# Kernel optimization log

Hardware: AMD Instinct MI355X
Metric: run time of the kernel (lower is better)

The kernel has to match this reference:

```python
import jax, jax.numpy as jnp
import numpy as np

EPS = 1e-8

def setup_inputs() -> dict:
    key = jax.random.key(0)
    k1, k2 = jax.random.split(key)
    B, N, D, K = 8, 8192, 768, 256
    x = jax.random.normal(k1, (B, N, D), dtype=jnp.float32)
    centers = jax.random.normal(k2, (B, K, D), dtype=jnp.float32)
    return {"x": x, "centers": centers}

def reference(x, centers):
    # tokens_norm / centers_norm as in the torch module (add-eps normalization)
    tn = x / (jnp.linalg.norm(x, axis=-1, keepdims=True) + EPS)
    cn = centers / (jnp.linalg.norm(centers, axis=-1, keepdims=True) + EPS)
    # F.cosine_similarity re-normalizes with clamp(norm, min=eps)
    tn2 = tn / jnp.maximum(jnp.linalg.norm(tn, axis=-1, keepdims=True), EPS)
    cn2 = cn / jnp.maximum(jnp.linalg.norm(cn, axis=-1, keepdims=True), EPS)
    # fused: cosine similarity via plain matmul instead of (B,N,K,D) broadcast
    cos_sim = jnp.einsum('bnd,bkd->bnk', tn2, cn2)  # (B,N,K)
    dist = 1.0 - cos_sim
    prob = jax.nn.softmax(-dist, axis=-1)  # softmax over K
    # weighted aggregation over N: (B,K,D)
    num = jnp.einsum('bnk,bnd->bkd', prob, x)
    den = jnp.sum(prob, axis=1)[..., None] + EPS  # (B,K,1)
    return num / den
```

## Files before the change

kernel.cpp:

```cpp
#include <hip/hip_runtime.h>
#include <hip/hip_bf16.h>

typedef __attribute__((ext_vector_type(8))) short bf16x8;
typedef __attribute__((ext_vector_type(4))) float f32x4;
typedef unsigned short u16;
typedef unsigned int u32;

__device__ __forceinline__ u16 f2bf(float f) {
    u32 u = __float_as_uint(f);
    u = (u + 0x7FFFu + ((u >> 16) & 1u)) >> 16;
    return (u16)u;
}
__device__ __forceinline__ u32 pk2(float a, float b) {
    return (u32)f2bf(a) | ((u32)f2bf(b) << 16);
}

#define GLDS16(g, l) __builtin_amdgcn_global_load_lds( \
    (const __attribute__((address_space(1))) u32*)(g), \
    (__attribute__((address_space(3))) u32*)(l), 16, 0, 0)

__global__ __launch_bounds__(256) void k_centers(const float* __restrict__ c, u16* __restrict__ cn,
                                                 float* __restrict__ den, float* __restrict__ out) {
    int bid = blockIdx.x;
    int w = threadIdx.x >> 6, lane = threadIdx.x & 63;
    int row = (bid << 2) + w;
    int b = row >> 8;
    if (bid < 8) den[(bid << 8) + threadIdx.x] = 0.f;
    {
        float4* o4 = reinterpret_cast<float4*>(out) + (size_t)bid * 768 + threadIdx.x;
        o4[0] = float4{0.f, 0.f, 0.f, 0.f};
        o4[256] = float4{0.f, 0.f, 0.f, 0.f};
        o4[512] = float4{0.f, 0.f, 0.f, 0.f};
    }
    __shared__ u16 rb[4][800];
    const float* src = c + (size_t)row * 768;
    float v[12]; float ss = 0.f;
#pragma unroll
    for (int j = 0; j < 12; ++j) { v[j] = src[lane + (j << 6)]; ss += v[j] * v[j]; }
#pragma unroll
    for (int m = 1; m < 64; m <<= 1) ss += __shfl_xor(ss, m, 64);
    float inv = 1.0f / sqrtf(ss);
#pragma unroll
    for (int j = 0; j < 12; ++j) rb[w][lane + (j << 6)] = f2bf(v[j] * inv);
    __syncthreads();
    int t = threadIdx.x;
    int k0 = (bid << 2) & 255;
#pragma unroll
    for (int p = 0; p < 2; ++p) {
        int idx = (p << 8) + t;
        if (idx < 384) {
            int g = idx >> 2, kr = idx & 3;
            uint4 val = *reinterpret_cast<const uint4*>(&rb[kr][g << 3]);
            int kb = g >> 2, dc = g & 3;
            size_t o = ((((size_t)(b * 24 + kb) << 2) + dc) << 8) + k0 + kr;
            *reinterpret_cast<uint4*>(cn + (o << 3)) = val;
        }
    }
}

__global__ __launch_bounds__(256, 2) void k_gemm1(const float* __restrict__ x, const u16* __restrict__ cn,
                                                  u16* __restrict__ probT, float* __restrict__ den) {
    const int b = blockIdx.y;
    const int n0 = blockIdx.x << 7;
    const int t = threadIdx.x;
    const int wave = t >> 6, lane = t & 63;
    const int lg = lane >> 4, lr = lane & 15;
    const int wm = wave >> 1, wk = wave & 1;
    const int tok0 = wm << 6;
    const int kb0 = wk << 7;

    __shared__ union {
        struct {
            u16 A[2][4][130][8];
            u16 B[2][4][256][8];
        } s;
        u16 T[256][136];
    } u;
    __shared__ float inv_s[128];
    __shared__ float ksum[2][128];
    __shared__ float denp[256];

    denp[t] = 0.f;

    f32x4 acc[8][4];
#pragma unroll
    for (int kf = 0; kf < 8; ++kf)
#pragma unroll
        for (int tf = 0; tf < 4; ++tf) acc[kf][tf] = (f32x4){0.f, 0.f, 0.f, 0.f};

    const char* cnb = (const char*)(cn + (size_t)b * 24 * 4 * 256 * 8);
    const int tokS = ((t >> 1) & 63) + ((t >> 7) << 6);
    const int dcS = t & 1;
    const float* ap = x + ((size_t)b * 8192 + n0 + tokS) * 768 + (dcS << 3);

    float sq = 0.f;
    float4 f0, f1, f2, f3;

    auto issueA = [&](int kb) {
        const float* p = ap + (kb << 5);
        f0 = *reinterpret_cast<const float4*>(p);
        f1 = *reinterpret_cast<const float4*>(p + 4);
        f2 = *reinterpret_cast<const float4*>(p + 16);
        f3 = *reinterpret_cast<const float4*>(p + 20);
    };
    auto writeA = [&](int buf) {
        sq += f0.x*f0.x + f0.y*f0.y + f0.z*f0.z + f0.w*f0.w
            + f1.x*f1.x + f1.y*f1.y + f1.z*f1.z + f1.w*f1.w
            + f2.x*f2.x + f2.y*f2.y + f2.z*f2.z + f2.w*f2.w
            + f3.x*f3.x + f3.y*f3.y + f3.z*f3.z + f3.w*f3.w;
        *reinterpret_cast<uint4*>(&u.s.A[buf][dcS][tokS][0]) =
            make_uint4(pk2(f0.x, f0.y), pk2(f0.z, f0.w), pk2(f1.x, f1.y), pk2(f1.z, f1.w));
        *reinterpret_cast<uint4*>(&u.s.A[buf][dcS + 2][tokS][0]) =
            make_uint4(pk2(f2.x, f2.y), pk2(f2.z, f2.w), pk2(f3.x, f3.y), pk2(f3.z, f3.w));
    };
    auto issueB = [&](int buf, int kb) {
        const char* src = cnb + (size_t)kb * 16384 + (wave << 12) + (lane << 4);
        char* dst = (char*)&u.s.B[buf][0][0][0] + (wave << 12);
        GLDS16(src, dst);
        GLDS16(src + 1024, dst + 1024);
        GLDS16(src + 2048, dst + 2048);
        GLDS16(src + 3072, dst + 3072);
    };

    issueA(0); issueB(0, 0);
    writeA(0);
    __syncthreads();

    for (int kb = 0; kb < 24; ++kb) {
        int cur = kb & 1, nxt = cur ^ 1;
        if (kb < 23) { issueA(kb + 1); issueB(nxt, kb + 1); }
        bf16x8 a[4];
#pragma unroll
        for (int tf = 0; tf < 4; ++tf)
            a[tf] = *reinterpret_cast<const bf16x8*>(&u.s.A[cur][lg][tok0 + (tf << 4) + lr][0]);
#pragma unroll
        for (int kf = 0; kf < 8; ++kf) {
            bf16x8 bb = *reinterpret_cast<const bf16x8*>(&u.s.B[cur][lg][kb0 + (kf << 4) + lr][0]);
#pragma unroll
            for (int tf = 0; tf < 4; ++tf)
                acc[kf][tf] = __builtin_amdgcn_mfma_f32_16x16x32_bf16(a[tf], bb, acc[kf][tf], 0, 0, 0);
        }
        if (kb < 23) writeA(nxt);
        __syncthreads();
    }

    sq += __shfl_xor(sq, 1, 64);
    if ((t & 1) == 0) inv_s[tokS] = 1.0f / sqrtf(sq);
    __syncthreads();

    float iv[4][4];
#pragma unroll
    for (int tf = 0; tf < 4; ++tf)
#pragma unroll
        for (int r = 0; r < 4; ++r)
            iv[tf][r] = inv_s[tok0 + (tf << 4) + (lg << 2) + r];

    float rowsum[4][4];
#pragma unroll
    for (int tf = 0; tf < 4; ++tf)
#pragma unroll
        for (int r = 0; r < 4; ++r) rowsum[tf][r] = 0.f;
#pragma unroll
    for (int kf = 0; kf < 8; ++kf)
#pragma unroll
        for (int tf = 0; tf < 4; ++tf)
#pragma unroll
            for (int r = 0; r < 4; ++r) {
                float e = __expf(acc[kf][tf][r] * iv[tf][r]);
                acc[kf][tf][r] = e; rowsum[tf][r] += e;
            }
#pragma unroll
    for (int tf = 0; tf < 4; ++tf)
#pragma unroll
        for (int r = 0; r < 4; ++r) {
#pragma unroll
            for (int m = 1; m < 16; m <<= 1) rowsum[tf][r] += __shfl_xor(rowsum[tf][r], m, 64);
        }
    if (lr == 0) {
#pragma unroll
        for (int tf = 0; tf < 4; ++tf)
#pragma unroll
            for (int r = 0; r < 4; ++r)
                ksum[wk][tok0 + (tf << 4) + (lg << 2) + r] = rowsum[tf][r];
    }
    __syncthreads();

    float rs[4][4];
#pragma unroll
    for (int tf = 0; tf < 4; ++tf)
#pragma unroll
        for (int r = 0; r < 4; ++r) {
            int idx = tok0 + (tf << 4) + (lg << 2) + r;
            rs[tf][r] = 1.0f / (ksum[0][idx] + ksum[1][idx]);
        }

    float dcol[8];
#pragma unroll
    for (int kf = 0; kf < 8; ++kf) dcol[kf] = 0.f;
#pragma unroll
    for (int kf = 0; kf < 8; ++kf)
#pragma unroll
        for (int tf = 0; tf < 4; ++tf)
#pragma unroll
            for (int r = 0; r < 4; ++r) {
                float p = acc[kf][tf][r] * rs[tf][r];
                acc[kf][tf][r] = p; dcol[kf] += p;
            }
#pragma unroll
    for (int kf = 0; kf < 8; ++kf) {
        dcol[kf] += __shfl_xor(dcol[kf], 16, 64);
        dcol[kf] += __shfl_xor(dcol[kf], 32, 64);
    }
    if (lg == 0) {
#pragma unroll
        for (int kf = 0; kf < 8; ++kf) atomicAdd(&denp[kb0 + (kf << 4) + lr], dcol[kf]);
    }
#pragma unroll
    for (int kf = 0; kf < 8; ++kf)
#pragma unroll
        for (int tf = 0; tf < 4; ++tf)
            *reinterpret_cast<ushort4*>(&u.T[kb0 + (kf << 4) + lr][tok0 + (tf << 4) + (lg << 2)]) =
                make_ushort4(f2bf(acc[kf][tf][0]), f2bf(acc[kf][tf][1]),
                             f2bf(acc[kf][tf][2]), f2bf(acc[kf][tf][3]));
    __syncthreads();

    u16* pTb = probT + (size_t)b * 256 * 8192 + n0;
#pragma unroll
    for (int i = 0; i < 16; ++i) {
        int idx = (i << 8) + t;
        int row = idx >> 4, ch = idx & 15;
        *reinterpret_cast<uint4*>(pTb + (size_t)row * 8192 + (ch << 3)) =
            *reinterpret_cast<const uint4*>(&u.T[row][ch << 3]);
    }
    atomicAdd(&den[(b << 8) + t], denp[t]);
}

__global__ __launch_bounds__(256) void k_gemm2(const float* __restrict__ x, const u16* __restrict__ probT,
                                               const float* __restrict__ den, float* __restrict__ out) {
    const int bid = blockIdx.x;
    const int xcd = bid & 7, slot = bid >> 3;
    const int orig = xcd * 96 + slot;
    const int dt = orig % 12, sb = orig / 12;
    const int s = sb >> 3, b = sb & 7;
    const int d0 = dt << 6;
    const int t = threadIdx.x;
    const int wave = t >> 6, lane = t & 63;
    const int lg = lane >> 4, lr = lane & 15;

    f32x4 acc[4][4];
#pragma unroll
    for (int m = 0; m < 4; ++m)
#pragma unroll
        for (int tt = 0; tt < 4; ++tt) acc[m][tt] = (f32x4){0.f, 0.f, 0.f, 0.f};

    const int n0 = s << 10;
    const u16* pA = probT + (size_t)b * 256 * 8192;
    const float* xB = x + (size_t)b * 8192 * 768;

    for (int kb = 0; kb < 32; ++kb) {
        int nbase = n0 + (kb << 5);
        bf16x8 a[4];
#pragma unroll
        for (int m = 0; m < 4; ++m) {
            int k = (wave << 6) + (m << 4) + lr;
            a[m] = *reinterpret_cast<const bf16x8*>(pA + (size_t)k * 8192 + nbase + (lg << 3));
        }
        const float* xr = xB + (size_t)(nbase + (lg << 3)) * 768 + d0 + lr;
        bf16x8 bb[4];
#pragma unroll
        for (int tt = 0; tt < 4; ++tt)
#pragma unroll
            for (int j = 0; j < 8; ++j) {
                float f = xr[(size_t)j * 768 + (tt << 4)];
                bb[tt][j] = (short)f2bf(f);
            }
#pragma unroll
        for (int m = 0; m < 4; ++m)
#pragma unroll
            for (int tt = 0; tt < 4; ++tt)
                acc[m][tt] = __builtin_amdgcn_mfma_f32_16x16x32_bf16(a[m], bb[tt], acc[m][tt], 0, 0, 0);
    }

    float* ob = out + (size_t)(b << 8) * 768;
#pragma unroll
    for (int m = 0; m < 4; ++m) {
        int kb_ = (wave << 6) + (m << 4) + (lg << 2);
#pragma unroll
        for (int reg = 0; reg < 4; ++reg) {
            float dv = 1.0f / (den[(b << 8) + kb_ + reg] + 1e-8f);
#pragma unroll
            for (int tt = 0; tt < 4; ++tt)
                unsafeAtomicAdd(&ob[(size_t)(kb_ + reg) * 768 + d0 + (tt << 4) + lr],
                                acc[m][tt][reg] * dv);
        }
    }
}

extern "C" void kernel_launch(void* const* d_in, const int* in_sizes, int n_in,
                              void* d_out, int out_size, void* d_ws, size_t ws_size,
                              hipStream_t stream) {
    const float* x = (const float*)d_in[0];
    const float* centers = (const float*)d_in[1];
    float* out = (float*)d_out;
    char* ws = (char*)d_ws;
    u16* cn       = (u16*)ws;
    u16* probT    = (u16*)(ws + 3145728);
    float* den    = (float*)(ws + 36700160);

    k_centers<<<512, 256, 0, stream>>>(centers, cn, den, out);
    k_gemm1<<<dim3(64, 8), 256, 0, stream>>>(x, cn, probT, den);
    k_gemm2<<<768, 256, 0, stream>>>(x, probT, den, out);
}
```

Before: 164.4 us.

## Replace double-buffered GEMM1 main loop with single-buffer 64-wide K steps

The 24-step double-buffered loop, which prefetched the next x tile and centers tile while computing the current one, is replaced by 12 single-buffered steps covering 64 elements of D each. Both LDS buffers now hold the two halves of one step. Each step loads 8 float4 per thread, stores them to LDS, synchronizes, then runs twice as many MFMAs per barrier. This halves the number of loop iterations and barriers and the x loads become wider and contiguous, but the overlap between global loads and MFMA work inside a block is lost. The kernel now relies on its two resident blocks per CU to hide load latency.

Measured after the change: 159.8 us (median of 2 runs). -2.8%, faster.

```diff
diff --git a/kernel.cpp b/kernel.cpp
--- a/kernel.cpp
+++ b/kernel.cpp
@@ -71,7 +71,7 @@
 
     __shared__ union {
         struct {
-            u16 A[2][4][130][8];
+            u16 A[8][130][8];
             u16 B[2][4][256][8];
         } s;
         u16 T[256][136];
@@ -91,56 +91,51 @@
     const char* cnb = (const char*)(cn + (size_t)b * 24 * 4 * 256 * 8);
     const int tokS = ((t >> 1) & 63) + ((t >> 7) << 6);
     const int dcS = t & 1;
-    const float* ap = x + ((size_t)b * 8192 + n0 + tokS) * 768 + (dcS << 3);
+    const float* ap = x + ((size_t)b * 8192 + n0 + tokS) * 768 + (dcS << 5);
 
     float sq = 0.f;
-    float4 f0, f1, f2, f3;
-
-    auto issueA = [&](int kb) {
-        const float* p = ap + (kb << 5);
-        f0 = *reinterpret_cast<const float4*>(p);
-        f1 = *reinterpret_cast<const float4*>(p + 4);
-        f2 = *reinterpret_cast<const float4*>(p + 16);
-        f3 = *reinterpret_cast<const float4*>(p + 20);
-    };
-    auto writeA = [&](int buf) {
-        sq += f0.x*f0.x + f0.y*f0.y + f0.z*f0.z + f0.w*f0.w
-            + f1.x*f1.x + f1.y*f1.y + f1.z*f1.z + f1.w*f1.w
-            + f2.x*f2.x + f2.y*f2.y + f2.z*f2.z + f2.w*f2.w
-            + f3.x*f3.x + f3.y*f3.y + f3.z*f3.z + f3.w*f3.w;
-        *reinterpret_cast<uint4*>(&u.s.A[buf][dcS][tokS][0]) =
-            make_uint4(pk2(f0.x, f0.y), pk2(f0.z, f0.w), pk2(f1.x, f1.y), pk2(f1.z, f1.w));
-        *reinterpret_cast<uint4*>(&u.s.A[buf][dcS + 2][tokS][0]) =
-            make_uint4(pk2(f2.x, f2.y), pk2(f2.z, f2.w), pk2(f3.x, f3.y), pk2(f3.z, f3.w));
-    };
-    auto issueB = [&](int buf, int kb) {
-        const char* src = cnb + (size_t)kb * 16384 + (wave << 12) + (lane << 4);
-        char* dst = (char*)&u.s.B[buf][0][0][0] + (wave << 12);
-        GLDS16(src, dst);
-        GLDS16(src + 1024, dst + 1024);
-        GLDS16(src + 2048, dst + 2048);
-        GLDS16(src + 3072, dst + 3072);
-    };
-
-    issueA(0); issueB(0, 0);
-    writeA(0);
-    __syncthreads();
-
-    for (int kb = 0; kb < 24; ++kb) {
-        int cur = kb & 1, nxt = cur ^ 1;
-        if (kb < 23) { issueA(kb + 1); issueB(nxt, kb + 1); }
-        bf16x8 a[4];
-#pragma unroll
-        for (int tf = 0; tf < 4; ++tf)
-            a[tf] = *reinterpret_cast<const bf16x8*>(&u.s.A[cur][lg][tok0 + (tf << 4) + lr][0]);
+
+    for (int it = 0; it < 12; ++it) {
+        const float* p = ap + (it << 6);
+        float4 f[8];
+#pragma unroll
+        for (int j = 0; j < 8; ++j) f[j] = *reinterpret_cast<const float4*>(p + (j << 2));
+#pragma unroll
+        for (int h = 0; h < 2; ++h) {
+            const char* src = cnb + (size_t)((it << 1) + h) * 16384 + (wave << 12) + (lane << 4);
+            char* dst = (char*)&u.s.B[h][0][0][0] + (wave << 12);
+            GLDS16(src, dst);
+            GLDS16(src + 1024, dst + 1024);
+            GLDS16(src + 2048, dst + 2048);
+            GLDS16(src + 3072, dst + 3072);
+        }
+#pragma unroll
+        for (int j = 0; j < 8; ++j)
+            sq += f[j].x * f[j].x + f[j].y * f[j].y + f[j].z * f[j].z + f[j].w * f[j].w;
+#pragma unroll
+        for (int j = 0; j < 4; ++j) {
+            *reinterpret_cast<uint4*>(&u.s.A[(dcS << 2) + j][tokS][0]) =
+                make_uint4(pk2(f[2 * j].x, f[2 * j].y), pk2(f[2 * j].z, f[2 * j].w),
+                           pk2(f[2 * j + 1].x, f[2 * j + 1].y), pk2(f[2 * j + 1].z, f[2 * j + 1].w));
+        }
+        __syncthreads();
+
+        bf16x8 a[4][2];
+#pragma unroll
+        for (int tf = 0; tf < 4; ++tf)
+#pragma unroll
+            for (int h = 0; h < 2; ++h)
+                a[tf][h] = *reinterpret_cast<const bf16x8*>(&u.s.A[(h << 2) + lg][tok0 + (tf << 4) + lr][0]);
 #pragma unroll
         for (int kf = 0; kf < 8; ++kf) {
-            bf16x8 bb = *reinterpret_cast<const bf16x8*>(&u.s.B[cur][lg][kb0 + (kf << 4) + lr][0]);
-#pragma unroll
-            for (int tf = 0; tf < 4; ++tf)
-                acc[kf][tf] = __builtin_amdgcn_mfma_f32_16x16x32_bf16(a[tf], bb, acc[kf][tf], 0, 0, 0);
-        }
-        if (kb < 23) writeA(nxt);
+#pragma unroll
+            for (int h = 0; h < 2; ++h) {
+                bf16x8 bb = *reinterpret_cast<const bf16x8*>(&u.s.B[h][lg][kb0 + (kf << 4) + lr][0]);
+#pragma unroll
+                for (int tf = 0; tf < 4; ++tf)
+                    acc[kf][tf] = __builtin_amdgcn_mfma_f32_16x16x32_bf16(a[tf][h], bb, acc[kf][tf], 0, 0, 0);
+            }
+        }
         __syncthreads();
     }
 
```
